# Kernel optimization log

Hardware: AMD Instinct MI355X
Metric: run time of the kernel (lower is better)

## Reference

```python
import jax, jax.numpy as jnp
import numpy as np
from jax import lax

# Problem sizes (see shape_source)
B, N, S, K = 16, 4096, 1024, 32   # clouds, points/cloud, fps samples/cloud, max neighbors
C_IN, H1, H2, C_OUT = 64, 64, 64, 128
R = 0.2                            # radius ball query radius


def setup_inputs() -> dict:
    key = jax.random.key(0)
    ks = jax.random.split(key, 6)
    x = jax.random.normal(ks[0], (B * N, C_IN), jnp.float32)
    pos = jax.random.uniform(ks[1], (B * N, 3), jnp.float32)  # unit cube
    batch = jnp.repeat(jnp.arange(B, dtype=jnp.int32), N)     # equal-size clouds
    def lin(k, fan_in, fan_out):
        return jax.random.normal(k, (fan_in, fan_out), jnp.float32) / np.float32(np.sqrt(fan_in))
    W1 = lin(ks[2], C_IN + 3, H1); b1 = jnp.zeros((H1,), jnp.float32)
    W2 = lin(ks[3], H1, H2);      b2 = jnp.zeros((H2,), jnp.float32)
    W3 = lin(ks[4], H2, C_OUT);   b3 = jnp.zeros((C_OUT,), jnp.float32)
    return dict(x=x, pos=pos, batch=batch, W1=W1, b1=b1, W2=W2, b2=b2, W3=W3, b3=b3)


def _fps_single(pos):
    """Farthest point sampling on one cloud. pos: [N,3] -> [S] int32 indices.
    Deterministic start at index 0 (random_start=False equivalent)."""
    def step(carry, _):
        mind, last = carry
        d = jnp.sum((pos - pos[last]) ** 2, axis=-1)   # [N]
        mind = jnp.minimum(mind, d)
        nxt = jnp.argmax(mind).astype(jnp.int32)
        return (mind, nxt), last
    init = (jnp.full((pos.shape[0],), jnp.inf, pos.dtype), jnp.int32(0))
    _, idx = lax.scan(step, init, None, length=S)
    return idx  # [S]


def _radius_single(pos, qpos):
    """Ball query: for each query return up to K in-radius neighbors (first K by
    point index, matching torch_cluster's 'first found' semantics).
    pos: [N,3], qpos: [S,3] -> (nbr [S,K] int32, mask [S,K] bool)."""
    d2 = jnp.sum((qpos[:, None, :] - pos[None, :, :]) ** 2, axis=-1)   # [S,N]
    valid = d2 <= R * R
    key = jnp.where(valid, jnp.arange(N, dtype=jnp.int32), jnp.int32(N))  # invalid -> sentinel N
    neg_key, nbr = lax.top_k(-key, K)        # K smallest keys == first K valid indices
    mask = (-neg_key) < N
    nbr = jnp.where(mask, nbr, 0).astype(jnp.int32)  # safe gather index
    return nbr, mask


def reference(x, pos, batch, W1, b1, W2, b2, W3, b3):
    xb = x.reshape(B, N, C_IN)
    posb = pos.reshape(B, N, 3)

    # 1) FPS sampling per cloud
    idx = jax.vmap(_fps_single)(posb)                                   # [B,S]
    qpos = jnp.take_along_axis(posb, idx[:, :, None], axis=1)           # [B,S,3]

    # 2) radius ball query (max 32 neighbors)
    nbr, mask = jax.vmap(_radius_single)(posb, qpos)                    # [B,S,K]

    # 3) PointNetConv: gather, relative pos, MLP, masked max-scatter
    flat = nbr.reshape(B, S * K)
    xj = jnp.take_along_axis(xb, flat[:, :, None], axis=1).reshape(B, S, K, C_IN)
    pj = jnp.take_along_axis(posb, flat[:, :, None], axis=1).reshape(B, S, K, 3)
    rel = pj - qpos[:, :, None, :]                                      # pos_j - pos_i
    h = jnp.concatenate([xj, rel], axis=-1)                             # [B,S,K,C_IN+3]
    h = jax.nn.relu(h @ W1 + b1)
    h = jax.nn.relu(h @ W2 + b2)
    h = h @ W3 + b3                                                     # [B,S,K,C_OUT]
    h = jnp.where(mask[..., None], h, -jnp.inf)
    agg = jnp.max(h, axis=2)                                            # max aggregation
    agg = jnp.where(jnp.any(mask, axis=2)[..., None], agg, 0.0)         # empty -> 0
    out = jax.nn.relu(agg)                                              # [B,S,C_OUT]

    new_batch = jnp.repeat(jnp.arange(B, dtype=batch.dtype), S)
    return out.reshape(B * S, C_OUT), qpos.reshape(B * S, 3), new_batch
```

## Files before the change

kernel.cpp:

```cpp
#include <hip/hip_runtime.h>
#include <cstdint>
#include <cstddef>

#define B_    16
#define N_    4096
#define S_    1024
#define K_    32
#define COUT_ 128
#define NQ_   (B_*S_)

#define FT 256
#define FP (N_/FT)

__device__ __forceinline__ uint64_t wave_max_u64(uint64_t key) {
  uint32_t lo = (uint32_t)key, hi = (uint32_t)(key >> 32);
#define DPP_STEP(ctrl) { \
    uint32_t lo2 = (uint32_t)__builtin_amdgcn_update_dpp((int)lo, (int)lo, (ctrl), 0xf, 0xf, false); \
    uint32_t hi2 = (uint32_t)__builtin_amdgcn_update_dpp((int)hi, (int)hi, (ctrl), 0xf, 0xf, false); \
    const bool gt = (hi2 > hi) || (hi2 == hi && lo2 > lo); \
    hi = gt ? hi2 : hi; lo = gt ? lo2 : lo; \
  }
  DPP_STEP(0x111)
  DPP_STEP(0x112)
  DPP_STEP(0x114)
  DPP_STEP(0x118)
  DPP_STEP(0x142)
  DPP_STEP(0x143)
#undef DPP_STEP
  hi = (uint32_t)__builtin_amdgcn_readlane((int)hi, 63);
  lo = (uint32_t)__builtin_amdgcn_readlane((int)lo, 63);
  return ((uint64_t)hi << 32) | lo;
}

__global__ __launch_bounds__(FT) void fps_kernel(
    const float* __restrict__ pos, float* __restrict__ qpos_out,
    float* __restrict__ batch_out)
{
  __shared__ float px[N_], py[N_], pz[N_];
  __shared__ int   hist[S_];
  __shared__ uint64_t wkeys[2][FT/64];

  const int t = threadIdx.x;
  const int blk = blockIdx.x;
  const float* pb = pos + (size_t)blk * N_ * 3;

  for (int i = t; i < N_; i += FT) {
    px[i] = pb[i*3+0]; py[i] = pb[i*3+1]; pz[i] = pb[i*3+2];
  }
  for (int s = t; s < S_; s += FT) batch_out[(size_t)blk*S_ + s] = (float)blk;
  __syncthreads();

  float rx[FP], ry[FP], rz[FP], mind[FP];
  #pragma unroll
  for (int k = 0; k < FP; ++k) {
    const int p = k*FT + t;
    rx[k] = px[p]; ry[k] = py[p]; rz[k] = pz[p];
    mind[k] = INFINITY;
  }

  int last = 0;
  for (int s = 0; s < S_; ++s) {
    if (t == 0) hist[s] = last;
    if (s == S_-1) break;
    const float lx = px[last], ly = py[last], lz = pz[last];
    uint64_t best = 0;
    #pragma unroll
    for (int k = 0; k < FP; ++k) {
      #pragma clang fp contract(off)
      const float dx = rx[k]-lx;
      const float dy = ry[k]-ly;
      const float dz = rz[k]-lz;
      const float d  = dx*dx + dy*dy + dz*dz;
      const float m  = fminf(mind[k], d);
      mind[k] = m;
      const uint64_t key = ((uint64_t)__float_as_uint(m) << 32)
                         | (uint32_t)((N_-1) - (k*FT + t));
      if (key > best) best = key;
    }
    best = wave_max_u64(best);
    if ((t & 63) == 0) wkeys[s & 1][t >> 6] = best;
    __syncthreads();
    uint64_t gb = wkeys[s & 1][0];
    #pragma unroll
    for (int w = 1; w < FT/64; ++w) {
      const uint64_t o = wkeys[s & 1][w];
      if (o > gb) gb = o;
    }
    last = (N_-1) - (int)(uint32_t)gb;
  }
  __syncthreads();
  for (int s = t; s < S_; s += FT) {
    const int p = hist[s];
    qpos_out[((size_t)blk*S_ + s)*3 + 0] = px[p];
    qpos_out[((size_t)blk*S_ + s)*3 + 1] = py[p];
    qpos_out[((size_t)blk*S_ + s)*3 + 2] = pz[p];
  }
}

__global__ __launch_bounds__(256) void radius_kernel(
    const float* __restrict__ pos, const float* __restrict__ qpos,
    int* __restrict__ nbr, int* __restrict__ cnt_out)
{
  const int lane = threadIdx.x & 63;
  const int q = blockIdx.x * 4 + (threadIdx.x >> 6);
  const int b = q >> 10;
  const float* pb = pos + (size_t)b * N_ * 3;
  const float qx = qpos[(size_t)q*3+0];
  const float qy = qpos[(size_t)q*3+1];
  const float qz = qpos[(size_t)q*3+2];
  int cnt = 0;
  for (int base = 0; base < N_; base += 64) {
    #pragma clang fp contract(off)
    const int i = base + lane;
    const float dx = qx - pb[i*3+0];
    const float dy = qy - pb[i*3+1];
    const float dz = qz - pb[i*3+2];
    const float d  = dx*dx + dy*dy + dz*dz;
    const bool valid = (d <= 0.04f);
    const unsigned long long bal = __ballot(valid);
    const int below = __popcll(bal & ((1ull << lane) - 1ull));
    const int p = cnt + below;
    if (valid && p < K_) nbr[(size_t)q*K_ + p] = i;
    cnt += __popcll(bal);
    if (cnt >= K_) break;
  }
  const int c = (cnt < K_) ? cnt : K_;
  if (lane >= c && lane < K_) nbr[(size_t)q*K_ + lane] = 0;
  if (lane == 0) cnt_out[q] = c;
}

__global__ __launch_bounds__(256) void xw_kernel(
    const float* __restrict__ x, const float* __restrict__ W1,
    float* __restrict__ xw)
{
  __shared__ float xs[64*65];
  __shared__ float ws[64*64];
  const int t = threadIdx.x;
  const size_t rowbase = (size_t)blockIdx.x * 64;
  for (int k = t; k < 4096; k += 256) {
    xs[(k >> 6)*65 + (k & 63)] = x[rowbase*64 + k];
    ws[k] = W1[k];
  }
  __syncthreads();
  const int rg = t >> 4, cg = t & 15;
  const int r0 = rg*4, c0 = cg*4;
  float acc[4][4] = {};
  for (int i = 0; i < 64; ++i) {
    const float4 w = *(const float4*)&ws[i*64 + c0];
    #pragma unroll
    for (int j = 0; j < 4; ++j) {
      const float a = xs[(r0+j)*65 + i];
      acc[j][0] = fmaf(a, w.x, acc[j][0]);
      acc[j][1] = fmaf(a, w.y, acc[j][1]);
      acc[j][2] = fmaf(a, w.z, acc[j][2]);
      acc[j][3] = fmaf(a, w.w, acc[j][3]);
    }
  }
  #pragma unroll
  for (int j = 0; j < 4; ++j) {
    float4 v; v.x=acc[j][0]; v.y=acc[j][1]; v.z=acc[j][2]; v.w=acc[j][3];
    *(float4*)&xw[(rowbase + r0 + j)*64 + c0] = v;
  }
}

__global__ __launch_bounds__(256) void conv_kernel(
    const float* __restrict__ pos, const float* __restrict__ qpos,
    const int* __restrict__ nbr, const int* __restrict__ cnt,
    const float* __restrict__ xw,
    const float* __restrict__ W1, const float* __restrict__ b1,
    const float* __restrict__ W2, const float* __restrict__ b2,
    const float* __restrict__ W3, const float* __restrict__ b3,
    float* __restrict__ out)
{
  __shared__ float h1s[64*68];
  __shared__ float h2s[64*68];
  __shared__ float red[8*128];
  __shared__ int   nbrs[64];
  __shared__ float qps[8];
  __shared__ int   cnts[2];

  const int t  = threadIdx.x;
  const int q0 = blockIdx.x * 2;
  const int b  = q0 >> 10;

  if (t < 64) nbrs[t] = nbr[(size_t)q0*K_ + t];
  if (t < 2)  cnts[t] = cnt[q0 + t];
  if (t < 6)  qps[(t/3)*4 + (t%3)] = qpos[(size_t)q0*3 + t];
  __syncthreads();

  {
    const int c = t & 63;
    const int rsub = t >> 6;
    const float w1x = W1[64*64 + c];
    const float w1y = W1[65*64 + c];
    const float w1z = W1[66*64 + c];
    const float b1v = b1[c];
    #pragma unroll
    for (int it = 0; it < 16; ++it) {
      const int row = it*4 + rsub;
      const int lq  = row >> 5;
      const int j   = nbrs[row];
      const size_t gp = (size_t)b*N_ + j;
      const float xv = xw[gp*64 + c];
      const float rx = pos[gp*3+0] - qps[lq*4+0];
      const float ry = pos[gp*3+1] - qps[lq*4+1];
      const float rz = pos[gp*3+2] - qps[lq*4+2];
      float h = fmaf(rx, w1x, xv);
      h = fmaf(ry, w1y, h);
      h = fmaf(rz, w1z, h);
      h += b1v;
      h1s[row*68 + c] = fmaxf(h, 0.0f);
    }
  }
  __syncthreads();

  {
    const int rg = t >> 4, cg = t & 15;
    const int r0 = rg*4, c0 = cg*4;
    float acc[4][4] = {};
    for (int i = 0; i < 64; i += 4) {
      float a[4][4];
      #pragma unroll
      for (int j = 0; j < 4; ++j)
        *(float4*)&a[j][0] = *(const float4*)&h1s[(r0+j)*68 + i];
      #pragma unroll
      for (int di = 0; di < 4; ++di) {
        const float4 w = *(const float4*)&W2[(i+di)*64 + c0];
        #pragma unroll
        for (int j = 0; j < 4; ++j) {
          const float av = a[j][di];
          acc[j][0] = fmaf(av, w.x, acc[j][0]);
          acc[j][1] = fmaf(av, w.y, acc[j][1]);
          acc[j][2] = fmaf(av, w.z, acc[j][2]);
          acc[j][3] = fmaf(av, w.w, acc[j][3]);
        }
      }
    }
    const float4 bb = *(const float4*)&b2[c0];
    #pragma unroll
    for (int j = 0; j < 4; ++j) {
      float4 v;
      v.x = fmaxf(acc[j][0] + bb.x, 0.0f);
      v.y = fmaxf(acc[j][1] + bb.y, 0.0f);
      v.z = fmaxf(acc[j][2] + bb.z, 0.0f);
      v.w = fmaxf(acc[j][3] + bb.w, 0.0f);
      *(float4*)&h2s[(r0+j)*68 + c0] = v;
    }
  }
  __syncthreads();

  {
    const int rg = t >> 5, cg = t & 31;
    const int r0 = rg*8, c0 = cg*4;
    const int lq = rg >> 2;
    const int cq = cnts[lq];
    float acc[8][4] = {};
    for (int i = 0; i < 64; i += 4) {
      float a[8][4];
      #pragma unroll
      for (int j = 0; j < 8; ++j)
        *(float4*)&a[j][0] = *(const float4*)&h2s[(r0+j)*68 + i];
      #pragma unroll
      for (int di = 0; di < 4; ++di) {
        const float4 w = *(const float4*)&W3[(size_t)(i+di)*128 + c0];
        #pragma unroll
        for (int j = 0; j < 8; ++j) {
          const float av = a[j][di];
          acc[j][0] = fmaf(av, w.x, acc[j][0]);
          acc[j][1] = fmaf(av, w.y, acc[j][1]);
          acc[j][2] = fmaf(av, w.z, acc[j][2]);
          acc[j][3] = fmaf(av, w.w, acc[j][3]);
        }
      }
    }
    float pm0=-INFINITY, pm1=-INFINITY, pm2=-INFINITY, pm3=-INFINITY;
    #pragma unroll
    for (int j = 0; j < 8; ++j) {
      const int n = (r0 + j) & 31;
      if (n < cq) {
        pm0 = fmaxf(pm0, acc[j][0]);
        pm1 = fmaxf(pm1, acc[j][1]);
        pm2 = fmaxf(pm2, acc[j][2]);
        pm3 = fmaxf(pm3, acc[j][3]);
      }
    }
    float4 v; v.x=pm0; v.y=pm1; v.z=pm2; v.w=pm3;
    *(float4*)&red[rg*128 + c0] = v;
  }
  __syncthreads();
  {
    const int q = t >> 7, c = t & 127;
    const int cq = cnts[q];
    float v = -INFINITY;
    #pragma unroll
    for (int j = 0; j < 4; ++j) v = fmaxf(v, red[(q*4+j)*128 + c]);
    v = (cq > 0) ? (v + b3[c]) : 0.0f;
    v = fmaxf(v, 0.0f);
    out[(size_t)(q0 + q)*COUT_ + c] = v;
  }
}

extern "C" void kernel_launch(void* const* d_in, const int* in_sizes, int n_in,
                              void* d_out, int out_size, void* d_ws, size_t ws_size,
                              hipStream_t stream) {
  const float* x   = (const float*)d_in[0];
  const float* pos = (const float*)d_in[1];
  const float* W1  = (const float*)d_in[3];
  const float* b1  = (const float*)d_in[4];
  const float* W2  = (const float*)d_in[5];
  const float* b2  = (const float*)d_in[6];
  const float* W3  = (const float*)d_in[7];
  const float* b3  = (const float*)d_in[8];

  float* out    = (float*)d_out;
  float* qpos   = out + (size_t)NQ_*COUT_;
  float* batchf = qpos + (size_t)NQ_*3;

  char* ws = (char*)d_ws;
  float* xw = (float*)ws;
  int* nbr  = (int*)(ws + (size_t)B_*N_*64*sizeof(float));
  int* cnt  = nbr + (size_t)NQ_*K_;

  hipLaunchKernelGGL(xw_kernel,     dim3((B_*N_)/64), dim3(256), 0, stream, x, W1, xw);
  hipLaunchKernelGGL(fps_kernel,    dim3(B_),         dim3(FT),  0, stream, pos, qpos, batchf);
  hipLaunchKernelGGL(radius_kernel, dim3(NQ_/4),      dim3(256), 0, stream, pos, qpos, nbr, cnt);
  hipLaunchKernelGGL(conv_kernel,   dim3(NQ_/2),      dim3(256), 0, stream,
                     pos, qpos, nbr, cnt, xw, W1, b1, W2, b2, W3, b3, out);
}
```

Measured before the change: 888.5 us.

## Fuse radius query into conv kernel and carry winner coords through FPS reduction

The ball query now runs inside the conv kernel: two waves per block each scan the cloud for one query and write neighbor indices straight to shared memory, so the separate radius kernel and its nbr/cnt global round trip go away. The FPS kernel no longer stages the cloud in shared memory. Each lane tracks its best point's coordinates and packs them alongside the argmax key, so the next center is read from the reduction slot instead of a dependent shared-memory lookup of px[last]. The cost is that the conv blocks' other two waves sit idle during the serial neighbor scan, and the scan no longer runs as its own well-occupied kernel.

```diff
diff --git a/kernel.cpp b/kernel.cpp
--- a/kernel.cpp
+++ b/kernel.cpp
@@ -8,126 +8,6 @@
 #define K_    32
 #define COUT_ 128
 #define NQ_   (B_*S_)
-
-#define FT 256
-#define FP (N_/FT)
-
-__device__ __forceinline__ uint64_t wave_max_u64(uint64_t key) {
-  uint32_t lo = (uint32_t)key, hi = (uint32_t)(key >> 32);
-#define DPP_STEP(ctrl) { \
-    uint32_t lo2 = (uint32_t)__builtin_amdgcn_update_dpp((int)lo, (int)lo, (ctrl), 0xf, 0xf, false); \
-    uint32_t hi2 = (uint32_t)__builtin_amdgcn_update_dpp((int)hi, (int)hi, (ctrl), 0xf, 0xf, false); \
-    const bool gt = (hi2 > hi) || (hi2 == hi && lo2 > lo); \
-    hi = gt ? hi2 : hi; lo = gt ? lo2 : lo; \
-  }
-  DPP_STEP(0x111)
-  DPP_STEP(0x112)
-  DPP_STEP(0x114)
-  DPP_STEP(0x118)
-  DPP_STEP(0x142)
-  DPP_STEP(0x143)
-#undef DPP_STEP
-  hi = (uint32_t)__builtin_amdgcn_readlane((int)hi, 63);
-  lo = (uint32_t)__builtin_amdgcn_readlane((int)lo, 63);
-  return ((uint64_t)hi << 32) | lo;
-}
-
-__global__ __launch_bounds__(FT) void fps_kernel(
-    const float* __restrict__ pos, float* __restrict__ qpos_out,
-    float* __restrict__ batch_out)
-{
-  __shared__ float px[N_], py[N_], pz[N_];
-  __shared__ int   hist[S_];
-  __shared__ uint64_t wkeys[2][FT/64];
-
-  const int t = threadIdx.x;
-  const int blk = blockIdx.x;
-  const float* pb = pos + (size_t)blk * N_ * 3;
-
-  for (int i = t; i < N_; i += FT) {
-    px[i] = pb[i*3+0]; py[i] = pb[i*3+1]; pz[i] = pb[i*3+2];
-  }
-  for (int s = t; s < S_; s += FT) batch_out[(size_t)blk*S_ + s] = (float)blk;
-  __syncthreads();
-
-  float rx[FP], ry[FP], rz[FP], mind[FP];
-  #pragma unroll
-  for (int k = 0; k < FP; ++k) {
-    const int p = k*FT + t;
-    rx[k] = px[p]; ry[k] = py[p]; rz[k] = pz[p];
-    mind[k] = INFINITY;
-  }
-
-  int last = 0;
-  for (int s = 0; s < S_; ++s) {
-    if (t == 0) hist[s] = last;
-    if (s == S_-1) break;
-    const float lx = px[last], ly = py[last], lz = pz[last];
-    uint64_t best = 0;
-    #pragma unroll
-    for (int k = 0; k < FP; ++k) {
-      #pragma clang fp contract(off)
-      const float dx = rx[k]-lx;
-      const float dy = ry[k]-ly;
-      const float dz = rz[k]-lz;
-      const float d  = dx*dx + dy*dy + dz*dz;
-      const float m  = fminf(mind[k], d);
-      mind[k] = m;
-      const uint64_t key = ((uint64_t)__float_as_uint(m) << 32)
-                         | (uint32_t)((N_-1) - (k*FT + t));
-      if (key > best) best = key;
-    }
-    best = wave_max_u64(best);
-    if ((t & 63) == 0) wkeys[s & 1][t >> 6] = best;
-    __syncthreads();
-    uint64_t gb = wkeys[s & 1][0];
-    #pragma unroll
-    for (int w = 1; w < FT/64; ++w) {
-      const uint64_t o = wkeys[s & 1][w];
-      if (o > gb) gb = o;
-    }
-    last = (N_-1) - (int)(uint32_t)gb;
-  }
-  __syncthreads();
-  for (int s = t; s < S_; s += FT) {
-    const int p = hist[s];
-    qpos_out[((size_t)blk*S_ + s)*3 + 0] = px[p];
-    qpos_out[((size_t)blk*S_ + s)*3 + 1] = py[p];
-    qpos_out[((size_t)blk*S_ + s)*3 + 2] = pz[p];
-  }
-}
-
-__global__ __launch_bounds__(256) void radius_kernel(
-    const float* __restrict__ pos, const float* __restrict__ qpos,
-    int* __restrict__ nbr, int* __restrict__ cnt_out)
-{
-  const int lane = threadIdx.x & 63;
-  const int q = blockIdx.x * 4 + (threadIdx.x >> 6);
-  const int b = q >> 10;
-  const float* pb = pos + (size_t)b * N_ * 3;
-  const float qx = qpos[(size_t)q*3+0];
-  const float qy = qpos[(size_t)q*3+1];
-  const float qz = qpos[(size_t)q*3+2];
-  int cnt = 0;
-  for (int base = 0; base < N_; base += 64) {
-    #pragma clang fp contract(off)
-    const int i = base + lane;
-    const float dx = qx - pb[i*3+0];
-    const float dy = qy - pb[i*3+1];
-    const float dz = qz - pb[i*3+2];
-    const float d  = dx*dx + dy*dy + dz*dz;
-    const bool valid = (d <= 0.04f);
-    const unsigned long long bal = __ballot(valid);
-    const int below = __popcll(bal & ((1ull << lane) - 1ull));
-    const int p = cnt + below;
-    if (valid && p < K_) nbr[(size_t)q*K_ + p] = i;
-    cnt += __popcll(bal);
-    if (cnt >= K_) break;
-  }
-  const int c = (cnt < K_) ? cnt : K_;
-  if (lane >= c && lane < K_) nbr[(size_t)q*K_ + lane] = 0;
-  if (lane == 0) cnt_out[q] = c;
-}
 
 __global__ __launch_bounds__(256) void xw_kernel(
     const float* __restrict__ x, const float* __restrict__ W1,
@@ -163,9 +43,101 @@
   }
 }
 
+#define FT 256
+#define FP (N_/FT)
+
+__device__ __forceinline__ uint64_t wave_max_u64_bcast(uint64_t key) {
+  uint32_t lo = (uint32_t)key, hi = (uint32_t)(key >> 32);
+#define DPP_STEP(ctrl) { \
+    uint32_t lo2 = (uint32_t)__builtin_amdgcn_update_dpp((int)lo, (int)lo, (ctrl), 0xf, 0xf, false); \
+    uint32_t hi2 = (uint32_t)__builtin_amdgcn_update_dpp((int)hi, (int)hi, (ctrl), 0xf, 0xf, false); \
+    const bool gt = (hi2 > hi) || (hi2 == hi && lo2 > lo); \
+    hi = gt ? hi2 : hi; lo = gt ? lo2 : lo; \
+  }
+  DPP_STEP(0x111)
+  DPP_STEP(0x112)
+  DPP_STEP(0x114)
+  DPP_STEP(0x118)
+  DPP_STEP(0x142)
+  DPP_STEP(0x143)
+#undef DPP_STEP
+  hi = (uint32_t)__builtin_amdgcn_readlane((int)hi, 63);
+  lo = (uint32_t)__builtin_amdgcn_readlane((int)lo, 63);
+  return ((uint64_t)hi << 32) | lo;
+}
+
+__global__ __launch_bounds__(FT) void fps_kernel(
+    const float* __restrict__ pos, float* __restrict__ qpos_out,
+    float* __restrict__ batch_out)
+{
+  __shared__ float hx[S_], hy[S_], hz[S_];
+  __shared__ uint4 wslot[2][4];
+  __shared__ float wslotz[2][4];
+
+  const int t = threadIdx.x;
+  const int wid = t >> 6;
+  const int b = blockIdx.x;
+  const float* pb = pos + (size_t)b * N_ * 3;
+
+  float rx[FP], ry[FP], rz[FP], mind[FP];
+  #pragma unroll
+  for (int k = 0; k < FP; ++k) {
+    const int p = k*FT + t;
+    rx[k] = pb[p*3+0]; ry[k] = pb[p*3+1]; rz[k] = pb[p*3+2];
+    mind[k] = INFINITY;
+  }
+  for (int s = t; s < S_; s += FT) batch_out[(size_t)b*S_ + s] = (float)b;
+
+  float lx = pb[0], ly = pb[1], lz = pb[2];
+
+  for (int s = 0; s < S_; ++s) {
+    if (t == 0) { hx[s] = lx; hy[s] = ly; hz[s] = lz; }
+    if (s == S_-1) break;
+
+    float bm = -1.0f; int bp = 0;
+    float bx = 0.0f, by = 0.0f, bz = 0.0f;
+    #pragma unroll
+    for (int k = 0; k < FP; ++k) {
+      #pragma clang fp contract(off)
+      const float dx = rx[k]-lx;
+      const float dy = ry[k]-ly;
+      const float dz = rz[k]-lz;
+      const float d  = dx*dx + dy*dy + dz*dz;
+      const float m  = fminf(mind[k], d);
+      mind[k] = m;
+      if (m > bm) { bm = m; bp = k*FT + t; bx = rx[k]; by = ry[k]; bz = rz[k]; }
+    }
+    const uint64_t key = ((uint64_t)__float_as_uint(bm) << 32)
+                       | (uint32_t)((N_-1) - bp);
+    const uint64_t g = wave_max_u64_bcast(key);
+    const int par = s & 1;
+    if (key == g) {
+      uint4 c; c.x = (uint32_t)g; c.y = (uint32_t)(g >> 32);
+      c.z = __float_as_uint(bx); c.w = __float_as_uint(by);
+      wslot[par][wid] = c;
+      wslotz[par][wid] = bz;
+    }
+    __syncthreads();
+    {
+      uint4 c0 = wslot[par][0], c1 = wslot[par][1];
+      uint4 c2 = wslot[par][2], c3 = wslot[par][3];
+      float z0 = wslotz[par][0], z1 = wslotz[par][1];
+      float z2 = wslotz[par][2], z3 = wslotz[par][3];
+      if (c1.y > c0.y || (c1.y == c0.y && c1.x > c0.x)) { c0 = c1; z0 = z1; }
+      if (c3.y > c2.y || (c3.y == c2.y && c3.x > c2.x)) { c2 = c3; z2 = z3; }
+      if (c2.y > c0.y || (c2.y == c0.y && c2.x > c0.x)) { c0 = c2; z0 = z2; }
+      lx = __uint_as_float(c0.z); ly = __uint_as_float(c0.w); lz = z0;
+    }
+  }
+  __syncthreads();
+  for (int s = t; s < S_; s += FT) {
+    const size_t o = ((size_t)b*S_ + s)*3;
+    qpos_out[o+0] = hx[s]; qpos_out[o+1] = hy[s]; qpos_out[o+2] = hz[s];
+  }
+}
+
 __global__ __launch_bounds__(256) void conv_kernel(
     const float* __restrict__ pos, const float* __restrict__ qpos,
-    const int* __restrict__ nbr, const int* __restrict__ cnt,
     const float* __restrict__ xw,
     const float* __restrict__ W1, const float* __restrict__ b1,
     const float* __restrict__ W2, const float* __restrict__ b2,
@@ -181,11 +153,36 @@
 
   const int t  = threadIdx.x;
   const int q0 = blockIdx.x * 2;
-  const int b  = q0 >> 10;
-
-  if (t < 64) nbrs[t] = nbr[(size_t)q0*K_ + t];
-  if (t < 2)  cnts[t] = cnt[q0 + t];
-  if (t < 6)  qps[(t/3)*4 + (t%3)] = qpos[(size_t)q0*3 + t];
+  const int bb = q0 >> 10;
+  const int wid = t >> 6, lane = t & 63;
+
+  if (wid < 2) {
+    const int q = q0 + wid;
+    const float* pb = pos + (size_t)bb * N_ * 3;
+    const float qx = qpos[(size_t)q*3+0];
+    const float qy = qpos[(size_t)q*3+1];
+    const float qz = qpos[(size_t)q*3+2];
+    int cnt = 0;
+    for (int base = 0; base < N_; base += 64) {
+      #pragma clang fp contract(off)
+      const int i = base + lane;
+      const float dx = qx - pb[i*3+0];
+      const float dy = qy - pb[i*3+1];
+      const float dz = qz - pb[i*3+2];
+      const float d  = dx*dx + dy*dy + dz*dz;
+      const bool valid = (d <= 0.04f);
+      const unsigned long long bal = __ballot(valid);
+      const int below = __popcll(bal & ((1ull << lane) - 1ull));
+      const int p = cnt + below;
+      if (valid && p < K_) nbrs[wid*K_ + p] = i;
+      cnt += __popcll(bal);
+      if (cnt >= K_) break;
+    }
+    const int c = (cnt < K_) ? cnt : K_;
+    if (lane >= c && lane < K_) nbrs[wid*K_ + lane] = 0;
+    if (lane == 0) cnts[wid] = c;
+  }
+  if (t < 6) qps[(t/3)*4 + (t%3)] = qpos[(size_t)q0*3 + t];
   __syncthreads();
 
   {
@@ -199,15 +196,15 @@
     for (int it = 0; it < 16; ++it) {
       const int row = it*4 + rsub;
       const int lq  = row >> 5;
-      const int j   = nbrs[row];
-      const size_t gp = (size_t)b*N_ + j;
+      const int jn  = nbrs[row];
+      const size_t gp = (size_t)bb*N_ + jn;
       const float xv = xw[gp*64 + c];
-      const float rx = pos[gp*3+0] - qps[lq*4+0];
-      const float ry = pos[gp*3+1] - qps[lq*4+1];
-      const float rz = pos[gp*3+2] - qps[lq*4+2];
-      float h = fmaf(rx, w1x, xv);
-      h = fmaf(ry, w1y, h);
-      h = fmaf(rz, w1z, h);
+      const float rxx = pos[gp*3+0] - qps[lq*4+0];
+      const float ryy = pos[gp*3+1] - qps[lq*4+1];
+      const float rzz = pos[gp*3+2] - qps[lq*4+2];
+      float h = fmaf(rxx, w1x, xv);
+      h = fmaf(ryy, w1y, h);
+      h = fmaf(rzz, w1z, h);
       h += b1v;
       h1s[row*68 + c] = fmaxf(h, 0.0f);
     }
@@ -221,30 +218,30 @@
     for (int i = 0; i < 64; i += 4) {
       float a[4][4];
       #pragma unroll
-      for (int j = 0; j < 4; ++j)
-        *(float4*)&a[j][0] = *(const float4*)&h1s[(r0+j)*68 + i];
+      for (int jj = 0; jj < 4; ++jj)
+        *(float4*)&a[jj][0] = *(const float4*)&h1s[(r0+jj)*68 + i];
       #pragma unroll
       for (int di = 0; di < 4; ++di) {
         const float4 w = *(const float4*)&W2[(i+di)*64 + c0];
         #pragma unroll
-        for (int j = 0; j < 4; ++j) {
-          const float av = a[j][di];
-          acc[j][0] = fmaf(av, w.x, acc[j][0]);
-          acc[j][1] = fmaf(av, w.y, acc[j][1]);
-          acc[j][2] = fmaf(av, w.z, acc[j][2]);
-          acc[j][3] = fmaf(av, w.w, acc[j][3]);
+        for (int jj = 0; jj < 4; ++jj) {
+          const float av = a[jj][di];
+          acc[jj][0] = fmaf(av, w.x, acc[jj][0]);
+          acc[jj][1] = fmaf(av, w.y, acc[jj][1]);
+          acc[jj][2] = fmaf(av, w.z, acc[jj][2]);
+          acc[jj][3] = fmaf(av, w.w, acc[jj][3]);
         }
       }
     }
-    const float4 bb = *(const float4*)&b2[c0];
-    #pragma unroll
-    for (int j = 0; j < 4; ++j) {
+    const float4 bbv = *(const float4*)&b2[c0];
+    #pragma unroll
+    for (int jj = 0; jj < 4; ++jj) {
       float4 v;
-      v.x = fmaxf(acc[j][0] + bb.x, 0.0f);
-      v.y = fmaxf(acc[j][1] + bb.y, 0.0f);
-      v.z = fmaxf(acc[j][2] + bb.z, 0.0f);
-      v.w = fmaxf(acc[j][3] + bb.w, 0.0f);
-      *(float4*)&h2s[(r0+j)*68 + c0] = v;
+      v.x = fmaxf(acc[jj][0] + bbv.x, 0.0f);
+      v.y = fmaxf(acc[jj][1] + bbv.y, 0.0f);
+      v.z = fmaxf(acc[jj][2] + bbv.z, 0.0f);
+      v.w = fmaxf(acc[jj][3] + bbv.w, 0.0f);
+      *(float4*)&h2s[(r0+jj)*68 + c0] = v;
     }
   }
   __syncthreads();
@@ -258,30 +255,30 @@
     for (int i = 0; i < 64; i += 4) {
       float a[8][4];
       #pragma unroll
-      for (int j = 0; j < 8; ++j)
-        *(float4*)&a[j][0] = *(const float4*)&h2s[(r0+j)*68 + i];
+      for (int jj = 0; jj < 8; ++jj)
+        *(float4*)&a[jj][0] = *(const float4*)&h2s[(r0+jj)*68 + i];
       #pragma unroll
       for (int di = 0; di < 4; ++di) {
         const float4 w = *(const float4*)&W3[(size_t)(i+di)*128 + c0];
         #pragma unroll
-        for (int j = 0; j < 8; ++j) {
-          const float av = a[j][di];
-          acc[j][0] = fmaf(av, w.x, acc[j][0]);
-          acc[j][1] = fmaf(av, w.y, acc[j][1]);
-          acc[j][2] = fmaf(av, w.z, acc[j][2]);
-          acc[j][3] = fmaf(av, w.w, acc[j][3]);
+        for (int jj = 0; jj < 8; ++jj) {
+          const float av = a[jj][di];
+          acc[jj][0] = fmaf(av, w.x, acc[jj][0]);
+          acc[jj][1] = fmaf(av, w.y, acc[jj][1]);
+          acc[jj][2] = fmaf(av, w.z, acc[jj][2]);
+          acc[jj][3] = fmaf(av, w.w, acc[jj][3]);
         }
       }
     }
     float pm0=-INFINITY, pm1=-INFINITY, pm2=-INFINITY, pm3=-INFINITY;
     #pragma unroll
-    for (int j = 0; j < 8; ++j) {
-      const int n = (r0 + j) & 31;
+    for (int jj = 0; jj < 8; ++jj) {
+      const int n = (r0 + jj) & 31;
       if (n < cq) {
-        pm0 = fmaxf(pm0, acc[j][0]);
-        pm1 = fmaxf(pm1, acc[j][1]);
-        pm2 = fmaxf(pm2, acc[j][2]);
-        pm3 = fmaxf(pm3, acc[j][3]);
+        pm0 = fmaxf(pm0, acc[jj][0]);
+        pm1 = fmaxf(pm1, acc[jj][1]);
+        pm2 = fmaxf(pm2, acc[jj][2]);
+        pm3 = fmaxf(pm3, acc[jj][3]);
       }
     }
     float4 v; v.x=pm0; v.y=pm1; v.z=pm2; v.w=pm3;
@@ -293,7 +290,7 @@
     const int cq = cnts[q];
     float v = -INFINITY;
     #pragma unroll
-    for (int j = 0; j < 4; ++j) v = fmaxf(v, red[(q*4+j)*128 + c]);
+    for (int jj = 0; jj < 4; ++jj) v = fmaxf(v, red[(q*4+jj)*128 + c]);
     v = (cq > 0) ? (v + b3[c]) : 0.0f;
     v = fmaxf(v, 0.0f);
     out[(size_t)(q0 + q)*COUT_ + c] = v;
@@ -316,14 +313,10 @@
   float* qpos   = out + (size_t)NQ_*COUT_;
   float* batchf = qpos + (size_t)NQ_*3;
 
-  char* ws = (char*)d_ws;
-  float* xw = (float*)ws;
-  int* nbr  = (int*)(ws + (size_t)B_*N_*64*sizeof(float));
-  int* cnt  = nbr + (size_t)NQ_*K_;
-
-  hipLaunchKernelGGL(xw_kernel,     dim3((B_*N_)/64), dim3(256), 0, stream, x, W1, xw);
-  hipLaunchKernelGGL(fps_kernel,    dim3(B_),         dim3(FT),  0, stream, pos, qpos, batchf);
-  hipLaunchKernelGGL(radius_kernel, dim3(NQ_/4),      dim3(256), 0, stream, pos, qpos, nbr, cnt);
-  hipLaunchKernelGGL(conv_kernel,   dim3(NQ_/2),      dim3(256), 0, stream,
-                     pos, qpos, nbr, cnt, xw, W1, b1, W2, b2, W3, b3, out);
-}
+  float* xw = (float*)d_ws;
+
+  hipLaunchKernelGGL(xw_kernel,   dim3((B_*N_)/64), dim3(256), 0, stream, x, W1, xw);
+  hipLaunchKernelGGL(fps_kernel,  dim3(B_),         dim3(FT),  0, stream, pos, qpos, batchf);
+  hipLaunchKernelGGL(conv_kernel, dim3(NQ_/2),      dim3(256), 0, stream,
+                     pos, qpos, xw, W1, b1, W2, b2, W3, b3, out);
+}
```

Result: slower. 1.229 ms (+38.4%).
